# Performance work log

Measured on AMD Instinct MI355X. Metric: run time of the kernel, lower is better.

## Reference

```python
import jax, jax.numpy as jnp
import numpy as np

NUM_GROUPS = 32
EPS = 1e-5
NUM_HEAD = 8
DIM_HEAD = 64


def group_norm(t, w, b):
    # t: (B, N, C) tokens; GroupNorm over (N, C//G) within each group
    B, N, C = t.shape
    g = t.reshape(B, N, NUM_GROUPS, C // NUM_GROUPS)
    mu = g.mean(axis=(1, 3), keepdims=True)
    var = g.var(axis=(1, 3), keepdims=True)
    g = (g - mu) * jax.lax.rsqrt(var + EPS)
    return g.reshape(B, N, C) * w + b


def setup_inputs() -> dict:
    key = jax.random.key(0)
    ks = jax.random.split(key, 4)
    B, C, H, W = 2, 512, 48, 48
    hidden = NUM_HEAD * DIM_HEAD
    return {
        "x": jax.random.normal(ks[0], (B, C, H, W), dtype=jnp.float32),
        "gn1_w": jnp.ones((C,), jnp.float32),
        "gn1_b": jnp.zeros((C,), jnp.float32),
        "w_qkv": jax.random.normal(ks[1], (3 * hidden, C), jnp.float32) * 0.02,
        "mem_kv": jax.random.normal(ks[2], (2, NUM_HEAD, DIM_HEAD, 4), jnp.float32),
        "w_out": jax.random.normal(ks[3], (C, hidden), jnp.float32) * 0.02,
        "b_out": jnp.zeros((C,), jnp.float32),
        "gn2_w": jnp.ones((C,), jnp.float32),
        "gn2_b": jnp.zeros((C,), jnp.float32),
    }


def reference(x, gn1_w, gn1_b, w_qkv, mem_kv, w_out, b_out, gn2_w, gn2_b):
    B, C, H, W = x.shape
    N = H * W
    hidden = NUM_HEAD * DIM_HEAD
    scale = DIM_HEAD ** -0.5

    # tokens: (B, N, C)
    t = x.reshape(B, C, N).transpose(0, 2, 1)
    t = group_norm(t, gn1_w, gn1_b)

    # 1x1 conv QKV projection == per-token GEMM
    qkv = t @ w_qkv.T  # (B, N, 3*hidden)
    q, k, v = jnp.split(qkv, 3, axis=-1)

    def to_heads(a):  # (B, N, hidden) -> (B, nh, N, dh)
        return a.reshape(B, N, NUM_HEAD, DIM_HEAD).transpose(0, 2, 1, 3)

    q, k, v = to_heads(q), to_heads(k), to_heads(v)

    # memory kv prepended along sequence axis: (nh, dh, nkv) -> (1, nh, nkv, dh)
    mk = jnp.broadcast_to(mem_kv[0].transpose(0, 2, 1)[None], (B, NUM_HEAD, mem_kv.shape[-1], DIM_HEAD))
    mv = jnp.broadcast_to(mem_kv[1].transpose(0, 2, 1)[None], (B, NUM_HEAD, mem_kv.shape[-1], DIM_HEAD))
    k = jnp.concatenate([mk, k], axis=2)
    v = jnp.concatenate([mv, v], axis=2)

    scores = jnp.einsum('bhid,bhjd->bhij', q, k) * scale  # (B, nh, N, N+nkv)
    attn = jax.nn.softmax(scores, axis=-1)  # dropout = identity in eval
    o = jnp.einsum('bhij,bhjd->bhid', attn, v)  # (B, nh, N, dh)

    o = o.transpose(0, 2, 1, 3).reshape(B, N, hidden)
    o = o @ w_out.T + b_out  # 1x1 out conv
    o = group_norm(o, gn2_w, gn2_b)
    return o.transpose(0, 2, 1).reshape(B, C, H, W)
```

## Files before the change

kernel.cpp:

```cpp
#include <hip/hip_runtime.h>
#include <hip/hip_bf16.h>

typedef short short8 __attribute__((ext_vector_type(8)));
typedef float f32x4 __attribute__((ext_vector_type(4)));

#define GPTR(x) ((const __attribute__((address_space(1))) void*)(x))
#define LPTR(x) ((__attribute__((address_space(3))) void*)(x))

static __device__ __forceinline__ unsigned short f2bf(float f) {
  __hip_bfloat16 h = __float2bfloat16(f);
  return __builtin_bit_cast(unsigned short, h);
}
static __device__ __forceinline__ float bf2f(unsigned short u) {
  unsigned int v = ((unsigned int)u) << 16;
  return __builtin_bit_cast(float, v);
}
static __device__ __forceinline__ float fexp2(float x) {
#if __has_builtin(__builtin_amdgcn_exp2f)
  return __builtin_amdgcn_exp2f(x);
#else
  return exp2f(x);
#endif
}
static __device__ __forceinline__ unsigned short bftrunc(float f) {
  return (unsigned short)(__builtin_bit_cast(unsigned int, f) >> 16);
}

static __device__ __forceinline__ void block_reduce2(float& s, float& q) {
#pragma unroll
  for (int o = 32; o > 0; o >>= 1) { s += __shfl_down(s, o); q += __shfl_down(q, o); }
  __shared__ float rs[4], rq[4];
  int tid = threadIdx.x;
  if ((tid & 63) == 0) { rs[tid >> 6] = s; rq[tid >> 6] = q; }
  __syncthreads();
  if (tid == 0) {
    s = rs[0] + rs[1] + rs[2] + rs[3];
    q = rq[0] + rq[1] + rq[2] + rq[3];
  }
}

__global__ __launch_bounds__(256) void gn1_stats_kernel(const float* __restrict__ x,
                                                        float2* __restrict__ part1) {
  int bgc = blockIdx.x;
  const float4* base = (const float4*)x + (size_t)bgc * 1152;
  float s = 0.f, q = 0.f;
  for (int i = threadIdx.x; i < 1152; i += 256) {
    float4 v = base[i];
    s += v.x + v.y + v.z + v.w;
    q += v.x * v.x + v.y * v.y + v.z * v.z + v.w * v.w;
  }
  block_reduce2(s, q);
  if (threadIdx.x == 0) part1[bgc] = make_float2(s, q);
}

__global__ __launch_bounds__(256) void tnorm_prep_kernel(const float* __restrict__ x,
    const float* __restrict__ gw, const float* __restrict__ gb,
    const float2* __restrict__ part1, unsigned short* __restrict__ t,
    const float* __restrict__ wqkv, const float* __restrict__ wout,
    const float* __restrict__ memkv,
    unsigned short* __restrict__ wq, unsigned short* __restrict__ wo,
    unsigned short* __restrict__ Kb, unsigned short* __restrict__ Vt) {
  __shared__ float tile[32][33];
  int blk = blockIdx.x;
  if (blk < 2304) {
    int n0 = (blk % 72) * 32, c0 = ((blk / 72) & 15) * 32, b = blk / 1152;
    int g0 = c0 >> 4;
    float mu2[2], rs2[2];
#pragma unroll
    for (int gg = 0; gg < 2; gg++) {
      float s = 0.f, q = 0.f;
      const float2* p = part1 + (size_t)(b * 32 + g0 + gg) * 8;
#pragma unroll
      for (int k = 0; k < 8; k++) { float2 v = p[k]; s += v.x; q += v.y; }
      float mu = s / 36864.f;
      float var = q / 36864.f - mu * mu;
      mu2[gg] = mu;
      rs2[gg] = rsqrtf(var + 1e-5f);
    }
    int tx = threadIdx.x & 31, ty = threadIdx.x >> 5;
#pragma unroll
    for (int r = 0; r < 4; r++) {
      int c = c0 + ty + r * 8;
      tile[ty + r * 8][tx] = x[((size_t)(b * 512 + c)) * 2304 + n0 + tx];
    }
    __syncthreads();
    int gg = tx >> 4;
#pragma unroll
    for (int r = 0; r < 4; r++) {
      int n = n0 + ty + r * 8;
      int c = c0 + tx;
      float v = tile[tx][ty + r * 8];
      t[((size_t)(b * 2304 + n)) * 512 + c] = f2bf((v - mu2[gg]) * rs2[gg] * gw[c] + gb[c]);
    }
  } else {
    int i = (blk - 2304) * 256 + threadIdx.x;
    if (i < 786432) {
      wq[i] = f2bf(wqkv[i]);
    } else if (i < 1048576) {
      int j = i - 786432;
      wo[j] = f2bf(wout[j]);
    } else if (i < 1056768) {
      int tt = i - 1048576;
      int d = tt & 63, j = (tt >> 6) & 3, h = (tt >> 8) & 7, b = (tt >> 11) & 1, s = tt >> 12;
      unsigned short bv = f2bf(memkv[((s * 8 + h) * 64 + d) * 4 + j]);
      if (s == 0) Kb[((size_t)(b * 8 + h) * 2308 + j) * 64 + d] = bv;
      else        Vt[((size_t)(b * 8 + h) * 64 + d) * 2368 + j] = bv;
    }
  }
}

__global__ __launch_bounds__(256) void gemm_qkv_kernel(
    const unsigned short* __restrict__ A, const unsigned short* __restrict__ Bw,
    unsigned short* __restrict__ Qb, unsigned short* __restrict__ Kb,
    unsigned short* __restrict__ Vt) {
  __shared__ __attribute__((aligned(16))) unsigned short As[64 * 32];
  __shared__ __attribute__((aligned(16))) unsigned short Bs[128 * 32];
  int m0 = blockIdx.x * 64, o0 = blockIdx.y * 128;
  int tid = threadIdx.x, lane = tid & 63, wave = tid >> 6;
  int quad = lane >> 4, l15 = lane & 15;
  int wm = wave & 1, wn = wave >> 1;
  const float CS = 0.18033688011112042f;
  f32x4 acc[2][4] = {};
  for (int k0 = 0; k0 < 512; k0 += 32) {
    __syncthreads();
    {
      int row = tid >> 2, cc = tid & 3;
      __builtin_amdgcn_global_load_lds(GPTR(A + (size_t)(m0 + row) * 512 + k0 + cc * 8),
                                       LPTR(As + tid * 8), 16, 0, 0);
    }
#pragma unroll
    for (int c = 0; c < 2; c++) {
      int q = tid + c * 256;
      int row = q >> 2, cc = q & 3;
      __builtin_amdgcn_global_load_lds(GPTR(Bw + (size_t)(o0 + row) * 512 + k0 + cc * 8),
                                       LPTR(Bs + q * 8), 16, 0, 0);
    }
    __syncthreads();
    short8 af[2], bf[4];
#pragma unroll
    for (int i = 0; i < 2; i++) af[i] = *(const short8*)(As + (wm * 32 + i * 16 + l15) * 32 + quad * 8);
#pragma unroll
    for (int j = 0; j < 4; j++) bf[j] = *(const short8*)(Bs + (wn * 64 + j * 16 + l15) * 32 + quad * 8);
#pragma unroll
    for (int i = 0; i < 2; i++)
#pragma unroll
      for (int j = 0; j < 4; j++)
        acc[i][j] = __builtin_amdgcn_mfma_f32_16x16x32_bf16(af[i], bf[j], acc[i][j], 0, 0, 0);
  }
#pragma unroll
  for (int i = 0; i < 2; i++) {
#pragma unroll
    for (int j = 0; j < 4; j++) {
      int colo = o0 + wn * 64 + j * 16 + l15;
      int part = colo >> 9, rr = colo & 511, h = rr >> 6, d = rr & 63;
      int mbase = m0 + wm * 32 + i * 16 + quad * 4;
      int b = (mbase >= 2304) ? 1 : 0;
      int n = mbase - b * 2304;
      if (part == 0) {
#pragma unroll
        for (int reg = 0; reg < 4; reg++)
          Qb[((size_t)(b * 8 + h) * 2304 + n + reg) * 64 + d] = f2bf(acc[i][j][reg] * CS);
      } else if (part == 1) {
#pragma unroll
        for (int reg = 0; reg < 4; reg++)
          Kb[((size_t)(b * 8 + h) * 2308 + 4 + n + reg) * 64 + d] = f2bf(acc[i][j][reg]);
      } else {
        unsigned short bv[4];
#pragma unroll
        for (int reg = 0; reg < 4; reg++) bv[reg] = f2bf(acc[i][j][reg]);
        unsigned long long pk = (unsigned long long)bv[0] | ((unsigned long long)bv[1] << 16) |
                                ((unsigned long long)bv[2] << 32) | ((unsigned long long)bv[3] << 48);
        *(unsigned long long*)(Vt + ((size_t)(b * 8 + h) * 64 + d) * 2368 + 4 + n) = pk;
      }
    }
  }
}

__global__ __launch_bounds__(256) void attn_kernel(
    const unsigned short* __restrict__ Qb, const unsigned short* __restrict__ Kb,
    const unsigned short* __restrict__ Vt,
    unsigned short* __restrict__ Opart, float* __restrict__ Lbuf) {
  __shared__ __attribute__((aligned(16))) unsigned short Ks[64 * 72];
  __shared__ __attribute__((aligned(16))) unsigned short Vts[64 * 72];
  __shared__ __attribute__((aligned(16))) unsigned short Ps[128 * 72];
  int qt = blockIdx.x, bh = blockIdx.y, sp = blockIdx.z;
  int m0 = qt * 128;
  int kt0 = sp * 10, kt1 = (kt0 + 10 < 37) ? kt0 + 10 : 37;
  const unsigned short* Qh = Qb + (size_t)bh * 2304 * 64;
  const unsigned short* Kh = Kb + (size_t)bh * 2308 * 64;
  const unsigned short* VtH = Vt + (size_t)bh * 64 * 2368;
  int tid = threadIdx.x, lane = tid & 63, wave = tid >> 6;
  int quad = lane >> 4, l15 = lane & 15;

  short8 qf[2][2];
#pragma unroll
  for (int i = 0; i < 2; i++)
#pragma unroll
    for (int s = 0; s < 2; s++)
      qf[i][s] = *(const short8*)(Qh + (size_t)(m0 + wave * 32 + i * 16 + l15) * 64 + s * 32 + quad * 8);

  f32x4 oacc[2][4] = {};
  float lsum[2][4] = {};

  for (int kt = kt0; kt < kt1; kt++) {
    __syncthreads();
#pragma unroll
    for (int c = 0; c < 2; c++) {
      int q = tid + c * 256;
      int krow = q >> 3, c8 = q & 7;
      int gk = kt * 64 + krow;
      uint4 kv = make_uint4(0, 0, 0, 0);
      if (gk < 2308) kv = *(const uint4*)(Kh + (size_t)gk * 64 + c8 * 8);
      *(uint4*)(Ks + krow * 72 + c8 * 8) = kv;
      uint4 vv = *(const uint4*)(VtH + (size_t)krow * 2368 + kt * 64 + c8 * 8);
      *(uint4*)(Vts + krow * 72 + c8 * 8) = vv;
    }
    __syncthreads();
    f32x4 sacc[2][4] = {};
#pragma unroll
    for (int s = 0; s < 2; s++) {
      short8 kf[4];
#pragma unroll
      for (int j = 0; j < 4; j++) kf[j] = *(const short8*)(Ks + (j * 16 + l15) * 72 + s * 32 + quad * 8);
#pragma unroll
      for (int i = 0; i < 2; i++)
#pragma unroll
        for (int j = 0; j < 4; j++)
          sacc[i][j] = __builtin_amdgcn_mfma_f32_16x16x32_bf16(qf[i][s], kf[j], sacc[i][j], 0, 0, 0);
    }
    if (kt == 36) {
#pragma unroll
      for (int j = 0; j < 4; j++) {
        bool ok = (kt * 64 + j * 16 + l15) < 2308;
        if (!ok) {
#pragma unroll
          for (int i = 0; i < 2; i++)
#pragma unroll
            for (int r = 0; r < 4; r++) sacc[i][j][r] = -1e30f;
        }
      }
    }
#pragma unroll
    for (int i = 0; i < 2; i++) {
#pragma unroll
      for (int r = 0; r < 4; r++) {
        int prow = (wave * 32 + i * 16 + quad * 4 + r) * 72;
#pragma unroll
        for (int j = 0; j < 4; j++) {
          float p = fexp2(sacc[i][j][r]);
          lsum[i][r] += p;
          Ps[prow + j * 16 + l15] = bftrunc(p);
        }
      }
    }
#pragma unroll
    for (int s = 0; s < 2; s++) {
      short8 ap[2];
#pragma unroll
      for (int i = 0; i < 2; i++)
        ap[i] = *(const short8*)(Ps + (wave * 32 + i * 16 + l15) * 72 + s * 32 + quad * 8);
#pragma unroll
      for (int jo = 0; jo < 4; jo++) {
        short8 bv = *(const short8*)(Vts + (jo * 16 + l15) * 72 + s * 32 + quad * 8);
#pragma unroll
        for (int i = 0; i < 2; i++)
          oacc[i][jo] = __builtin_amdgcn_mfma_f32_16x16x32_bf16(ap[i], bv, oacc[i][jo], 0, 0, 0);
      }
    }
  }
#pragma unroll
  for (int i = 0; i < 2; i++)
#pragma unroll
    for (int r = 0; r < 4; r++) {
      float v = lsum[i][r];
#pragma unroll
      for (int o = 1; o < 16; o <<= 1) v += __shfl_xor(v, o);
      lsum[i][r] = v;
    }
  size_t obase = (size_t)(sp * 16 + bh) * 2304;
#pragma unroll
  for (int i = 0; i < 2; i++) {
#pragma unroll
    for (int r = 0; r < 4; r++) {
      int row = m0 + wave * 32 + i * 16 + quad * 4 + r;
#pragma unroll
      for (int jo = 0; jo < 4; jo++)
        Opart[(obase + row) * 64 + jo * 16 + l15] = f2bf(oacc[i][jo][r]);
      if (l15 == 0) Lbuf[obase + row] = lsum[i][r];
    }
  }
}

__global__ __launch_bounds__(256) void combine_kernel(
    const unsigned short* __restrict__ Opart, const float* __restrict__ Lbuf,
    unsigned short* __restrict__ Ot, float* __restrict__ p2s, float* __restrict__ p2q) {
  int t = threadIdx.x;
  if (blockIdx.x == 0 && t < 128) {
    if (t < 64) p2s[t] = 0.f;
    else        p2q[t - 64] = 0.f;
  }
  int rg = blockIdx.x * 16 + (t >> 4);
  int d4 = (t & 15) * 4;
  int bh = rg / 2304, row = rg - bh * 2304;
  int b = bh >> 3, h = bh & 7;
  float den = 0.f, num[4] = {};
#pragma unroll
  for (int s = 0; s < 4; s++) {
    size_t ri = ((size_t)(s * 16 + bh) * 2304 + row);
    den += Lbuf[ri];
    uint2 pv = *(const uint2*)(Opart + ri * 64 + d4);
    const unsigned short* pp = (const unsigned short*)&pv;
#pragma unroll
    for (int k = 0; k < 4; k++) num[k] += bf2f(pp[k]);
  }
  float rinv = 1.f / den;
  unsigned short ov[4];
#pragma unroll
  for (int k = 0; k < 4; k++) ov[k] = f2bf(num[k] * rinv);
  *(uint2*)(Ot + ((size_t)(b * 2304 + row)) * 512 + h * 64 + d4) = *(uint2*)ov;
}

__global__ __launch_bounds__(256) void gemm_out_kernel(
    const unsigned short* __restrict__ A, const unsigned short* __restrict__ Bw,
    const float* __restrict__ bias, float* __restrict__ y,
    float* __restrict__ p2s, float* __restrict__ p2q) {
  __shared__ __attribute__((aligned(16))) unsigned short As[64 * 32];
  __shared__ __attribute__((aligned(16))) unsigned short Bs[128 * 32];
  __shared__ float sgrp[8], qgrp[8];
  int m0 = blockIdx.x * 64, o0 = blockIdx.y * 128;
  int tid = threadIdx.x, lane = tid & 63, wave = tid >> 6;
  int quad = lane >> 4, l15 = lane & 15;
  int wm = wave & 1, wn = wave >> 1;
  if (tid < 8) { sgrp[tid] = 0.f; qgrp[tid] = 0.f; }
  f32x4 acc[2][4] = {};
  for (int k0 = 0; k0 < 512; k0 += 32) {
    __syncthreads();
    {
      int row = tid >> 2, cc = tid & 3;
      __builtin_amdgcn_global_load_lds(GPTR(A + (size_t)(m0 + row) * 512 + k0 + cc * 8),
                                       LPTR(As + tid * 8), 16, 0, 0);
    }
#pragma unroll
    for (int c = 0; c < 2; c++) {
      int q = tid + c * 256;
      int row = q >> 2, cc = q & 3;
      __builtin_amdgcn_global_load_lds(GPTR(Bw + (size_t)(o0 + row) * 512 + k0 + cc * 8),
                                       LPTR(Bs + q * 8), 16, 0, 0);
    }
    __syncthreads();
    short8 af[2], bf[4];
#pragma unroll
    for (int i = 0; i < 2; i++) af[i] = *(const short8*)(As + (wm * 32 + i * 16 + l15) * 32 + quad * 8);
#pragma unroll
    for (int j = 0; j < 4; j++) bf[j] = *(const short8*)(Bs + (wn * 64 + j * 16 + l15) * 32 + quad * 8);
#pragma unroll
    for (int i = 0; i < 2; i++)
#pragma unroll
      for (int j = 0; j < 4; j++)
        acc[i][j] = __builtin_amdgcn_mfma_f32_16x16x32_bf16(af[i], bf[j], acc[i][j], 0, 0, 0);
  }
  float ss[4] = {}, qq[4] = {};
#pragma unroll
  for (int i = 0; i < 2; i++) {
#pragma unroll
    for (int j = 0; j < 4; j++) {
      int colo = o0 + wn * 64 + j * 16 + l15;
      float bb = bias[colo];
#pragma unroll
      for (int reg = 0; reg < 4; reg++) {
        int m = m0 + wm * 32 + i * 16 + quad * 4 + reg;
        float v = acc[i][j][reg] + bb;
        y[(size_t)m * 512 + colo] = v;
        ss[j] += v;
        qq[j] += v * v;
      }
    }
  }
#pragma unroll
  for (int j = 0; j < 4; j++) {
#pragma unroll
    for (int o = 1; o < 64; o <<= 1) { ss[j] += __shfl_xor(ss[j], o); qq[j] += __shfl_xor(qq[j], o); }
  }
  if (lane == 0) {
#pragma unroll
    for (int j = 0; j < 4; j++) {
      atomicAdd(&sgrp[wn * 4 + j], ss[j]);
      atomicAdd(&qgrp[wn * 4 + j], qq[j]);
    }
  }
  __syncthreads();
  if (tid < 8) {
    int b = (m0 >= 2304) ? 1 : 0;
    int g = b * 32 + (o0 >> 4) + tid;
    atomicAdd(&p2s[g], sgrp[tid]);
    atomicAdd(&p2q[g], qgrp[tid]);
  }
}

__global__ __launch_bounds__(256) void gn2_final_kernel(const float* __restrict__ y,
    const float* __restrict__ gw, const float* __restrict__ gb,
    const float* __restrict__ p2s, const float* __restrict__ p2q,
    float* __restrict__ out) {
  __shared__ float tile[32][33];
  int n0 = blockIdx.x * 32, c0 = blockIdx.y * 32, b = blockIdx.z;
  int g0 = c0 >> 4;
  float mu2[2], rs2[2];
#pragma unroll
  for (int gg = 0; gg < 2; gg++) {
    float s = p2s[b * 32 + g0 + gg], q = p2q[b * 32 + g0 + gg];
    float mu = s / 36864.f;
    float var = q / 36864.f - mu * mu;
    mu2[gg] = mu;
    rs2[gg] = rsqrtf(var + 1e-5f);
  }
  int tx = threadIdx.x & 31, ty = threadIdx.x >> 5;
#pragma unroll
  for (int r = 0; r < 4; r++) {
    int n = n0 + ty + r * 8;
    tile[ty + r * 8][tx] = y[((size_t)(b * 2304 + n)) * 512 + c0 + tx];
  }
  __syncthreads();
#pragma unroll
  for (int r = 0; r < 4; r++) {
    int c = c0 + ty + r * 8;
    int gg = (ty + r * 8) >> 4;
    float v = tile[tx][ty + r * 8];
    out[((size_t)(b * 512 + c)) * 2304 + n0 + tx] = (v - mu2[gg]) * rs2[gg] * gw[c] + gb[c];
  }
}

extern "C" void kernel_launch(void* const* d_in, const int* in_sizes, int n_in,
                              void* d_out, int out_size, void* d_ws, size_t ws_size,
                              hipStream_t stream) {
  const float* x     = (const float*)d_in[0];
  const float* gn1w  = (const float*)d_in[1];
  const float* gn1b  = (const float*)d_in[2];
  const float* wqkv  = (const float*)d_in[3];
  const float* memkv = (const float*)d_in[4];
  const float* wout  = (const float*)d_in[5];
  const float* bout  = (const float*)d_in[6];
  const float* gn2w  = (const float*)d_in[7];
  const float* gn2b  = (const float*)d_in[8];
  float* out = (float*)d_out;

  char* ws = (char*)d_ws;
  float2* part1        = (float2*)(ws + 0);
  float* p2s           = (float*)(ws + 4096);
  float* p2q           = (float*)(ws + 4352);
  unsigned short* wqB  = (unsigned short*)(ws + 69632);
  unsigned short* woB  = (unsigned short*)(ws + 1642496);
  unsigned short* tB   = (unsigned short*)(ws + 2166784);
  unsigned short* Qb   = (unsigned short*)(ws + 6885376);
  unsigned short* Kb   = (unsigned short*)(ws + 11603968);
  unsigned short* Ot   = (unsigned short*)(ws + 21057536);
  float* y             = (float*)(ws + 25776128);
  unsigned short* Vt   = (unsigned short*)(ws + 35213312);
  unsigned short* Opart= (unsigned short*)(ws + 40062976);
  float* Lbuf          = (float*)(ws + 58937344);

  gn1_stats_kernel<<<512, 256, 0, stream>>>(x, part1);
  tnorm_prep_kernel<<<6432, 256, 0, stream>>>(x, gn1w, gn1b, part1, tB,
                                              wqkv, wout, memkv, wqB, woB, Kb, Vt);
  gemm_qkv_kernel<<<dim3(72, 12), 256, 0, stream>>>(tB, wqB, Qb, Kb, Vt);
  attn_kernel<<<dim3(18, 16, 4), 256, 0, stream>>>(Qb, Kb, Vt, Opart, Lbuf);
  combine_kernel<<<2304, 256, 0, stream>>>(Opart, Lbuf, Ot, p2s, p2q);
  gemm_out_kernel<<<dim3(72, 4), 256, 0, stream>>>(Ot, woB, bout, y, p2s, p2q);
  gn2_final_kernel<<<dim3(72, 16, 2), 256, 0, stream>>>(y, gn2w, gn2b, p2s, p2q, out);
}
```

Baseline: 168.2 us.

## Compute transposed scores so P stays in registers for PV MFMA

The attention kernel now computes S^T = K·Q^T, which puts each lane's probabilities in the layout the 16x16x16 bf16 MFMA expects as its A operand. P no longer has to go through shared memory, so the Ps buffer and its LDS writes and reads are gone. V is read as 4-element fragments from a re-padded tile. The row-sum reduction is simplified to two cross-quad shuffles. The trade-off is that PV now uses the smaller K=16 MFMA, issuing twice as many instructions, and the boundary masking moves into the exp loop.

Result: faster. 161.6 us (-3.9%).

```diff
diff --git a/kernel.cpp b/kernel.cpp
--- a/kernel.cpp
+++ b/kernel.cpp
@@ -2,6 +2,7 @@
 #include <hip/hip_bf16.h>
 
 typedef short short8 __attribute__((ext_vector_type(8)));
+typedef short short4b __attribute__((ext_vector_type(4)));
 typedef float f32x4 __attribute__((ext_vector_type(4)));
 
 #define GPTR(x) ((const __attribute__((address_space(1))) void*)(x))
@@ -22,8 +23,8 @@
   return exp2f(x);
 #endif
 }
-static __device__ __forceinline__ unsigned short bftrunc(float f) {
-  return (unsigned short)(__builtin_bit_cast(unsigned int, f) >> 16);
+static __device__ __forceinline__ short bftrunc(float f) {
+  return (short)(__builtin_bit_cast(unsigned int, f) >> 16);
 }
 
 static __device__ __forceinline__ void block_reduce2(float& s, float& q) {
@@ -181,8 +182,7 @@
     const unsigned short* __restrict__ Vt,
     unsigned short* __restrict__ Opart, float* __restrict__ Lbuf) {
   __shared__ __attribute__((aligned(16))) unsigned short Ks[64 * 72];
-  __shared__ __attribute__((aligned(16))) unsigned short Vts[64 * 72];
-  __shared__ __attribute__((aligned(16))) unsigned short Ps[128 * 72];
+  __shared__ __attribute__((aligned(16))) unsigned short Vts[64 * 68];
   int qt = blockIdx.x, bh = blockIdx.y, sp = blockIdx.z;
   int m0 = qt * 128;
   int kt0 = sp * 10, kt1 = (kt0 + 10 < 37) ? kt0 + 10 : 37;
@@ -200,7 +200,7 @@
       qf[i][s] = *(const short8*)(Qh + (size_t)(m0 + wave * 32 + i * 16 + l15) * 64 + s * 32 + quad * 8);
 
   f32x4 oacc[2][4] = {};
-  float lsum[2][4] = {};
+  float lsumT[2] = {};
 
   for (int kt = kt0; kt < kt1; kt++) {
     __syncthreads();
@@ -213,80 +213,58 @@
       if (gk < 2308) kv = *(const uint4*)(Kh + (size_t)gk * 64 + c8 * 8);
       *(uint4*)(Ks + krow * 72 + c8 * 8) = kv;
       uint4 vv = *(const uint4*)(VtH + (size_t)krow * 2368 + kt * 64 + c8 * 8);
-      *(uint4*)(Vts + krow * 72 + c8 * 8) = vv;
-    }
-    __syncthreads();
-    f32x4 sacc[2][4] = {};
-#pragma unroll
-    for (int s = 0; s < 2; s++) {
-      short8 kf[4];
-#pragma unroll
-      for (int j = 0; j < 4; j++) kf[j] = *(const short8*)(Ks + (j * 16 + l15) * 72 + s * 32 + quad * 8);
-#pragma unroll
-      for (int i = 0; i < 2; i++)
-#pragma unroll
-        for (int j = 0; j < 4; j++)
-          sacc[i][j] = __builtin_amdgcn_mfma_f32_16x16x32_bf16(qf[i][s], kf[j], sacc[i][j], 0, 0, 0);
-    }
-    if (kt == 36) {
-#pragma unroll
-      for (int j = 0; j < 4; j++) {
-        bool ok = (kt * 64 + j * 16 + l15) < 2308;
-        if (!ok) {
-#pragma unroll
-          for (int i = 0; i < 2; i++)
-#pragma unroll
-            for (int r = 0; r < 4; r++) sacc[i][j][r] = -1e30f;
+      *(uint4*)(Vts + krow * 68 + c8 * 8) = vv;
+    }
+    __syncthreads();
+    short4b pt[4][2];
+#pragma unroll
+    for (int jn = 0; jn < 4; jn++) {
+      f32x4 st[2] = {};
+#pragma unroll
+      for (int s = 0; s < 2; s++) {
+        short8 kf = *(const short8*)(Ks + (jn * 16 + l15) * 72 + s * 32 + quad * 8);
+#pragma unroll
+        for (int im = 0; im < 2; im++)
+          st[im] = __builtin_amdgcn_mfma_f32_16x16x32_bf16(kf, qf[im][s], st[im], 0, 0, 0);
+      }
+#pragma unroll
+      for (int im = 0; im < 2; im++) {
+#pragma unroll
+        for (int r = 0; r < 4; r++) {
+          float p = fexp2(st[im][r]);
+          if (kt == 36 && (jn * 16 + quad * 4 + r) >= 4) p = 0.f;
+          lsumT[im] += p;
+          pt[jn][im][r] = bftrunc(p);
         }
       }
     }
 #pragma unroll
-    for (int i = 0; i < 2; i++) {
-#pragma unroll
-      for (int r = 0; r < 4; r++) {
-        int prow = (wave * 32 + i * 16 + quad * 4 + r) * 72;
-#pragma unroll
-        for (int j = 0; j < 4; j++) {
-          float p = fexp2(sacc[i][j][r]);
-          lsum[i][r] += p;
-          Ps[prow + j * 16 + l15] = bftrunc(p);
-        }
+    for (int jn = 0; jn < 4; jn++) {
+#pragma unroll
+      for (int jo = 0; jo < 4; jo++) {
+        short4b vf = *(const short4b*)(Vts + (jo * 16 + l15) * 68 + jn * 16 + quad * 4);
+#pragma unroll
+        for (int im = 0; im < 2; im++)
+          oacc[im][jo] = __builtin_amdgcn_mfma_f32_16x16x16bf16_1k(pt[jn][im], vf, oacc[im][jo], 0, 0, 0);
       }
     }
-#pragma unroll
-    for (int s = 0; s < 2; s++) {
-      short8 ap[2];
-#pragma unroll
-      for (int i = 0; i < 2; i++)
-        ap[i] = *(const short8*)(Ps + (wave * 32 + i * 16 + l15) * 72 + s * 32 + quad * 8);
-#pragma unroll
-      for (int jo = 0; jo < 4; jo++) {
-        short8 bv = *(const short8*)(Vts + (jo * 16 + l15) * 72 + s * 32 + quad * 8);
-#pragma unroll
-        for (int i = 0; i < 2; i++)
-          oacc[i][jo] = __builtin_amdgcn_mfma_f32_16x16x32_bf16(ap[i], bv, oacc[i][jo], 0, 0, 0);
-      }
-    }
-  }
-#pragma unroll
-  for (int i = 0; i < 2; i++)
+  }
+  size_t obase = (size_t)(sp * 16 + bh) * 2304;
+#pragma unroll
+  for (int im = 0; im < 2; im++) {
+    float v = lsumT[im];
+    v += __shfl_xor(v, 16);
+    v += __shfl_xor(v, 32);
+    if (quad == 0) Lbuf[obase + m0 + wave * 32 + im * 16 + l15] = v;
+  }
+#pragma unroll
+  for (int im = 0; im < 2; im++) {
 #pragma unroll
     for (int r = 0; r < 4; r++) {
-      float v = lsum[i][r];
-#pragma unroll
-      for (int o = 1; o < 16; o <<= 1) v += __shfl_xor(v, o);
-      lsum[i][r] = v;
-    }
-  size_t obase = (size_t)(sp * 16 + bh) * 2304;
-#pragma unroll
-  for (int i = 0; i < 2; i++) {
-#pragma unroll
-    for (int r = 0; r < 4; r++) {
-      int row = m0 + wave * 32 + i * 16 + quad * 4 + r;
+      int row = m0 + wave * 32 + im * 16 + quad * 4 + r;
 #pragma unroll
       for (int jo = 0; jo < 4; jo++)
-        Opart[(obase + row) * 64 + jo * 16 + l15] = f2bf(oacc[i][jo][r]);
-      if (l15 == 0) Lbuf[obase + row] = lsum[i][r];
+        Opart[(obase + row) * 64 + jo * 16 + l15] = f2bf(oacc[im][jo][r]);
     }
   }
 }
```
